# Kernel tuning notes

Measured on AMD Instinct MI355X. Metric: run time of the kernel, lower is better.

Reference implementation:

```python
import jax, jax.numpy as jnp
import numpy as np

N_NODES = 10000
N_EDGES = 320000
N_GRAPHS = 64
K = 10
IN_C, HID_C, OUT_C = 128, 256, 128


def setup_inputs() -> dict:
    key = jax.random.key(0)
    ks = jax.random.split(key, 10)
    s_in = 1.0 / np.sqrt(IN_C)
    s_hid = 1.0 / np.sqrt(HID_C)
    return {
        "x": jax.random.normal(ks[0], (N_NODES, IN_C), jnp.float32),
        "W0": jax.random.normal(ks[1], (K, IN_C, HID_C), jnp.float32) * s_in,
        "b0": jnp.zeros((HID_C,), jnp.float32),
        "W1": jax.random.normal(ks[2], (K, HID_C, HID_C), jnp.float32) * s_hid,
        "b1": jnp.zeros((HID_C,), jnp.float32),
        "W2": jax.random.normal(ks[3], (K, HID_C, HID_C), jnp.float32) * s_hid,
        "b2": jnp.zeros((HID_C,), jnp.float32),
        "W_out": jax.random.normal(ks[4], (HID_C, OUT_C), jnp.float32) * s_hid,
        "b_out": jnp.zeros((OUT_C,), jnp.float32),
        "edge_index": jax.random.randint(ks[5], (2, N_EDGES), 0, N_NODES, jnp.int64),
        "batch": jnp.sort(jax.random.randint(ks[6], (N_NODES,), 0, N_GRAPHS, jnp.int64)),
    }


def _edge_norm(src, dst, n):
    # Scaled Laplacian L_hat = 2L/lambda_max - I with lambda_max=2 and sym norm
    # => L_hat = -D^{-1/2} A D^{-1/2} (diagonal entries cancel to 0).
    deg = jnp.zeros((n,), jnp.float32).at[src].add(1.0)
    dis = jnp.where(deg > 0, jax.lax.rsqrt(jnp.maximum(deg, 1.0)), 0.0)
    return -dis[src] * dis[dst]


def _propagate(x, src, dst, w, n):
    # message = w * x[src], aggregated by sum at dst
    return jax.ops.segment_sum(w[:, None] * x[src], dst, num_segments=n)


def _cheb_conv(x, src, dst, w, W, b, n):
    # Tx_0 = x; Tx_1 = L_hat x; Tx_k = 2 L_hat Tx_{k-1} - Tx_{k-2}
    K_ = W.shape[0]
    Tx0 = x
    out = Tx0 @ W[0]
    Tx1 = _propagate(Tx0, src, dst, w, n)
    out = out + Tx1 @ W[1]
    for k in range(2, K_):
        Tx2 = 2.0 * _propagate(Tx1, src, dst, w, n) - Tx0
        out = out + Tx2 @ W[k]
        Tx0, Tx1 = Tx1, Tx2
    return out + b


def reference(x, W0, b0, W1, b1, W2, b2, W_out, b_out, edge_index, batch):
    n = x.shape[0]
    src, dst = edge_index[0], edge_index[1]
    w = _edge_norm(src, dst, n)
    # 3 ChebConv layers, each followed by ReLU (norm=None, dropout=0)
    h = jax.nn.relu(_cheb_conv(x, src, dst, w, W0, b0, n))
    h = jax.nn.relu(_cheb_conv(h, src, dst, w, W1, b1, n))
    h = jax.nn.relu(_cheb_conv(h, src, dst, w, W2, b2, n))
    # global_mean_pool over batch ids
    sums = jax.ops.segment_sum(h, batch, num_segments=N_GRAPHS)
    cnts = jax.ops.segment_sum(jnp.ones((n,), h.dtype), batch, num_segments=N_GRAPHS)
    pooled = sums / jnp.maximum(cnts, 1.0)[:, None]
    return pooled @ W_out + b_out
```

## Files before the change

### kernel.cpp

```cpp
#include <hip/hip_runtime.h>
#include <cstdint>
#include <cstddef>

#define N_NODES 10000
#define N_EDGES 320000
#define N_GRAPHS 64
#define KCHEB 10
#define C_IN 128
#define C_HID 256
#define C_OUTC 128
#define POOL_CHUNK 40

static inline size_t align_up(size_t v, size_t a){ return (v + a - 1) / a * a; }

typedef __attribute__((ext_vector_type(8))) _Float16 half8;
typedef __attribute__((ext_vector_type(2))) _Float16 h2;
typedef __attribute__((ext_vector_type(4))) float f32x4;


__global__ void k_deg(const int* __restrict__ src, const int* __restrict__ dst,
                      int* __restrict__ deg, int* __restrict__ indeg){
  int e = blockIdx.x*blockDim.x + threadIdx.x;
  if(e < N_EDGES){
    atomicAdd(&deg[src[e]], 1);
    atomicAdd(&indeg[dst[e]], 1);
  }
}

__global__ __launch_bounds__(1024) void k_scan(const int* __restrict__ cnt,
                                               int* __restrict__ offs,
                                               int* __restrict__ cursor,
                                               const int* __restrict__ deg,
                                               float* __restrict__ dis){
  __shared__ int part[1024];
  const int n = N_NODES;
  const int CH = (n + 1023) / 1024;
  int tid = threadIdx.x;
  int base = tid * CH;
  int s = 0;
  for(int i = 0; i < CH; i++){
    int idx = base + i;
    if(idx < n){
      s += cnt[idx];
      int d = deg[idx];
      dis[idx] = d > 0 ? rsqrtf((float)d) : 0.f;
    }
  }
  part[tid] = s;
  __syncthreads();
  for(int off = 1; off < 1024; off <<= 1){
    int v = (tid >= off) ? part[tid - off] : 0;
    __syncthreads();
    part[tid] += v;
    __syncthreads();
  }
  int run = (tid == 0) ? 0 : part[tid - 1];
  for(int i = 0; i < CH; i++){
    int idx = base + i;
    if(idx < n){
      offs[idx] = run;
      cursor[idx] = run;
      run += cnt[idx];
    }
  }
  if(tid == 1023) offs[n] = part[1023];
}

__global__ void k_scatter(const int* __restrict__ src, const int* __restrict__ dst,
                          const float* __restrict__ dis, int* __restrict__ cursor,
                          int* __restrict__ csr_s, unsigned* __restrict__ csr_wp){
  int e = blockIdx.x*blockDim.x + threadIdx.x;
  if(e < N_EDGES){
    int s = src[e], d = dst[e];
    float w = -dis[s] * dis[d];
    unsigned short wb = __builtin_bit_cast(unsigned short, (_Float16)w);
    int p = atomicAdd(&cursor[d], 1);
    csr_s[p] = s;
    csr_wp[p] = (unsigned)wb * 0x00010001u;
  }
}

__global__ __launch_bounds__(128) void k_gbounds(const int* __restrict__ batch,
                                                 int* __restrict__ gstart,
                                                 int* __restrict__ gcnt){
  int g = threadIdx.x;
  if(g <= N_GRAPHS){
    int lo = 0, hi = N_NODES;
    while(lo < hi){
      int mid = (lo + hi) >> 1;
      if(batch[mid] < g) lo = mid + 1; else hi = mid;
    }
    gstart[g] = lo;
  }
  __syncthreads();
  if(g < N_GRAPHS) gcnt[g] = gstart[g + 1] - gstart[g];
}


__device__ inline void hfma4(h2* a, uint4 v, unsigned wbits){
  h2 w2 = __builtin_bit_cast(h2, wbits);
  a[0] += __builtin_bit_cast(h2, v.x) * w2;
  a[1] += __builtin_bit_cast(h2, v.y) * w2;
  a[2] += __builtin_bit_cast(h2, v.z) * w2;
  a[3] += __builtin_bit_cast(h2, v.w) * w2;
}

__global__ __launch_bounds__(256) void k_prop256h(const _Float16* __restrict__ Xb,
                                                  const _Float16* __restrict__ Pb,
                                                  _Float16* __restrict__ tx,
                                                  const int* __restrict__ csr_s,
                                                  const unsigned* __restrict__ csr_wp,
                                                  const int* __restrict__ offs,
                                                  float alpha){
  const int stride  = KCHEB * C_HID;
  const int strideB = stride * 2;
  int bid  = blockIdx.x;
  int half = (bid >> 2) & 1;
  int lh   = (bid >> 3) * 4 + (bid & 3);
  int l15  = threadIdx.x & 15;
  int lane = threadIdx.x & 63;
  int b16  = lane & 48;
  int e8   = l15 & 7;
  int node = lh * 16 + (threadIdx.x >> 4);
  if(node >= N_NODES) return;
  int j0 = offs[node], j1 = offs[node + 1];
  h2 a[4] = {};
  const char* __restrict__ gbase = (const char*)Xb + (half * (C_HID/2) + l15 * 8) * 2;
  int j = j0;
  int sv = 0; unsigned wv = 0;
  bool have = (j + 7 < j1);
  if(have){ sv = csr_s[j + e8] * strideB; wv = csr_wp[j + e8]; }
  while(have){
    int jn = j + 8;
    bool more = (jn + 7 < j1);
    int sv2 = 0; unsigned wv2 = 0;
    if(more){ sv2 = csr_s[jn + e8] * strideB; wv2 = csr_wp[jn + e8]; }
    uint4 v[8];
#pragma unroll
    for(int i = 0; i < 8; i++){
      int si = __shfl(sv, b16 + i);
      v[i] = *(const uint4*)(gbase + si);
    }
#pragma unroll
    for(int i = 0; i < 8; i++){
      unsigned wi = (unsigned)__shfl((int)wv, b16 + i);
      hfma4(a, v[i], wi);
    }
    sv = sv2; wv = wv2; j = jn; have = more;
  }
  for(; j < j1; j++){
    int si = csr_s[j] * strideB;
    uint4 v0 = *(const uint4*)(gbase + si);
    hfma4(a, v0, csr_wp[j]);
  }
  _Float16 ah = (_Float16)alpha;
  h2 al = {ah, ah};
  h2 r[4];
#pragma unroll
  for(int i = 0; i < 4; i++) r[i] = a[i] * al;
  size_t off = (size_t)node * stride + half * (C_HID/2) + l15 * 8;
  if(Pb){
    uint4 pv = *(const uint4*)(Pb + off);
    r[0] -= __builtin_bit_cast(h2, pv.x);
    r[1] -= __builtin_bit_cast(h2, pv.y);
    r[2] -= __builtin_bit_cast(h2, pv.z);
    r[3] -= __builtin_bit_cast(h2, pv.w);
  }
  uint4 ob;
  ob.x = __builtin_bit_cast(unsigned, r[0]);
  ob.y = __builtin_bit_cast(unsigned, r[1]);
  ob.z = __builtin_bit_cast(unsigned, r[2]);
  ob.w = __builtin_bit_cast(unsigned, r[3]);
  *(uint4*)(tx + off) = ob;
}

__global__ __launch_bounds__(256) void k_prop128(const _Float16* __restrict__ Xb,
                                                 const _Float16* __restrict__ Pb,
                                                 _Float16* __restrict__ tx,
                                                 const int* __restrict__ csr_s,
                                                 const unsigned* __restrict__ csr_wp,
                                                 const int* __restrict__ offs,
                                                 float alpha){
  const int stride  = KCHEB * C_IN;
  const int strideB = stride * 2;
  int hl   = threadIdx.x & 31;
  int b32  = threadIdx.x & 32;
  int e8   = hl & 7;
  int node = blockIdx.x * 8 + (threadIdx.x >> 5);
  int j0 = offs[node], j1 = offs[node + 1];
  h2 a[2] = {};
  const char* __restrict__ gbase = (const char*)Xb + hl * 8;
  int j = j0;
  int sv = 0; unsigned wv = 0;
  bool have = (j + 7 < j1);
  if(have){ sv = csr_s[j + e8] * strideB; wv = csr_wp[j + e8]; }
  while(have){
    int jn = j + 8;
    bool more = (jn + 7 < j1);
    int sv2 = 0; unsigned wv2 = 0;
    if(more){ sv2 = csr_s[jn + e8] * strideB; wv2 = csr_wp[jn + e8]; }
    uint2 v[8];
#pragma unroll
    for(int i = 0; i < 8; i++){
      int si = __shfl(sv, b32 + i);
      v[i] = *(const uint2*)(gbase + si);
    }
#pragma unroll
    for(int i = 0; i < 8; i++){
      unsigned wi = (unsigned)__shfl((int)wv, b32 + i);
      h2 w2 = __builtin_bit_cast(h2, wi);
      a[0] += __builtin_bit_cast(h2, v[i].x) * w2;
      a[1] += __builtin_bit_cast(h2, v[i].y) * w2;
    }
    sv = sv2; wv = wv2; j = jn; have = more;
  }
  for(; j < j1; j++){
    int si = csr_s[j] * strideB;
    h2 w2 = __builtin_bit_cast(h2, csr_wp[j]);
    uint2 v0 = *(const uint2*)(gbase + si);
    a[0] += __builtin_bit_cast(h2, v0.x) * w2;
    a[1] += __builtin_bit_cast(h2, v0.y) * w2;
  }
  _Float16 ah = (_Float16)alpha;
  h2 al = {ah, ah};
  h2 r0 = a[0] * al, r1 = a[1] * al;
  size_t off = (size_t)node * stride + hl * 4;
  if(Pb){
    uint2 pv = *(const uint2*)(Pb + off);
    r0 -= __builtin_bit_cast(h2, pv.x);
    r1 -= __builtin_bit_cast(h2, pv.y);
  }
  uint2 ob;
  ob.x = __builtin_bit_cast(unsigned, r0);
  ob.y = __builtin_bit_cast(unsigned, r1);
  *(uint2*)(tx + off) = ob;
}

template<int C>
__global__ void k_f2h(const float* __restrict__ X, _Float16* __restrict__ tx,
                      int tx_stride){
  int idx = blockIdx.x * blockDim.x + threadIdx.x;
  const int GPR = C / 4;
  if(idx < N_NODES * GPR){
    int r = idx / GPR;
    int c = (idx - r * GPR) * 4;
    float4 v = *(const float4*)(X + (size_t)r * C + c);
    h2 p0 = {(_Float16)v.x, (_Float16)v.y};
    h2 p1 = {(_Float16)v.z, (_Float16)v.w};
    uint2 ob;
    ob.x = __builtin_bit_cast(unsigned, p0);
    ob.y = __builtin_bit_cast(unsigned, p1);
    *(uint2*)(tx + (size_t)r * tx_stride + c) = ob;
  }
}

__global__ __launch_bounds__(256) void k_wt3t(const float* __restrict__ W0, _Float16* __restrict__ WT0,
                                              const float* __restrict__ W1, _Float16* __restrict__ WT1,
                                              const float* __restrict__ W2, _Float16* __restrict__ WT2){
  __shared__ float t[32][33];
  int b = blockIdx.x;
  const float* W; _Float16* WT; int R; int tb;
  if(b < 320){ W = W0; WT = WT0; R = 1280; tb = b; }
  else if(b < 960){ W = W1; WT = WT1; R = 2560; tb = b - 320; }
  else { W = W2; WT = WT2; R = 2560; tb = b - 960; }
  int tr = tb >> 3, tc = tb & 7;
  int tx = threadIdx.x & 31, ty = threadIdx.x >> 5;
#pragma unroll
  for(int i = 0; i < 4; i++){
    int r = tr * 32 + ty + 8 * i;
    t[ty + 8 * i][tx] = W[(size_t)r * 256 + tc * 32 + tx];
  }
  __syncthreads();
#pragma unroll
  for(int i = 0; i < 4; i++){
    int o = tc * 32 + ty + 8 * i;
    WT[(size_t)o * R + tr * 32 + tx] = (_Float16)t[tx][ty + 8 * i];
  }
}


__global__ __launch_bounds__(256) void k_gemm_f(const _Float16* __restrict__ A,
                                                const _Float16* __restrict__ BT,
                                                const float* __restrict__ bias,
                                                float* __restrict__ H,
                                                _Float16* __restrict__ tx2,
                                                int M, int Ktot){
  int b = blockIdx.x;
  int xcd = b & 7;
  int l = b >> 3;
  int m = xcd + 8 * (l >> 2);
  int n = l & 3;
  if(m * 128 >= M) return;
  int row0 = m * 128, col0 = n * 64;

  __shared__ short As[2][128 * 64];
  __shared__ short Bs[2][64 * 64];
  int tid = threadIdx.x;
  int lane = tid & 63;
  int wave = tid >> 6;
  int l15 = lane & 15;
  int quad = lane >> 4;
  int wm = (wave & 1) * 64;
  int wn = (wave >> 1) * 32;

  int ar[4], ag[4], asw[4], agr[4];
#pragma unroll
  for(int i = 0; i < 4; i++){
    int e = tid + 256 * i;
    ar[i] = e >> 3; ag[i] = e & 7;
    agr[i] = row0 + ar[i];
    asw[i] = ar[i] * 64 + ((ag[i] ^ (ar[i] & 7)) * 8);
  }
  int br[2], bg[2], bsw[2];
#pragma unroll
  for(int i = 0; i < 2; i++){
    int e = tid + 256 * i;
    br[i] = e >> 3; bg[i] = e & 7;
    bsw[i] = br[i] * 64 + ((bg[i] ^ (br[i] & 7)) * 8);
  }

  f32x4 acc[4][2] = {};
  uint4 av[4], bv[2];

  auto load = [&](int k0){
#pragma unroll
    for(int i = 0; i < 4; i++)
      av[i] = (agr[i] < M) ? *(const uint4*)(A + (size_t)agr[i] * Ktot + k0 + ag[i] * 8)
                           : make_uint4(0u, 0u, 0u, 0u);
#pragma unroll
    for(int i = 0; i < 2; i++)
      bv[i] = *(const uint4*)(BT + (size_t)(col0 + br[i]) * Ktot + k0 + bg[i] * 8);
  };
  auto stor = [&](int buf){
#pragma unroll
    for(int i = 0; i < 4; i++) *(uint4*)(&As[buf][asw[i]]) = av[i];
#pragma unroll
    for(int i = 0; i < 2; i++) *(uint4*)(&Bs[buf][bsw[i]]) = bv[i];
  };

  load(0);
  stor(0);
  __syncthreads();
  int nk = Ktot >> 6;
  for(int it = 0; it < nk; it++){
    int cur = it & 1;
    if(it + 1 < nk) load((it + 1) << 6);
#pragma unroll
    for(int kk = 0; kk < 64; kk += 32){
      int g = (kk >> 3) + quad;
      half8 a[4], bb[2];
#pragma unroll
      for(int mi = 0; mi < 4; mi++){
        int r = wm + mi * 16 + l15;
        a[mi] = *(const half8*)(&As[cur][r * 64 + ((g ^ (r & 7)) * 8)]);
      }
#pragma unroll
      for(int ni = 0; ni < 2; ni++){
        int nn = wn + ni * 16 + l15;
        bb[ni] = *(const half8*)(&Bs[cur][nn * 64 + ((g ^ (nn & 7)) * 8)]);
      }
#pragma unroll
      for(int mi = 0; mi < 4; mi++)
#pragma unroll
        for(int ni = 0; ni < 2; ni++)
          acc[mi][ni] = __builtin_amdgcn_mfma_f32_16x16x32_f16(a[mi], bb[ni], acc[mi][ni], 0, 0, 0);
    }
    if(it + 1 < nk){
      stor(cur ^ 1);
      __syncthreads();
    }
  }

  const int K256 = KCHEB * C_HID;
#pragma unroll
  for(int mi = 0; mi < 4; mi++){
#pragma unroll
    for(int ni = 0; ni < 2; ni++){
      int gcol = col0 + wn + ni * 16 + l15;
      float bvv = bias[gcol];
#pragma unroll
      for(int r = 0; r < 4; r++){
        int grow = row0 + wm + mi * 16 + quad * 4 + r;
        if(grow < M){
          float v = fmaxf(acc[mi][ni][r] + bvv, 0.f);
          if(tx2) tx2[(size_t)grow * K256 + gcol] = (_Float16)v;
          else    H[(size_t)grow * C_HID + gcol] = v;
        }
      }
    }
  }
}


__global__ __launch_bounds__(256) void k_pool2(const float* __restrict__ h,
                                               const int* __restrict__ batch,
                                               float* __restrict__ gsum){
  int c  = threadIdx.x;
  int n0 = blockIdx.x * POOL_CHUNK;
  int n1 = n0 + POOL_CHUNK;
  if(n1 > N_NODES) n1 = N_NODES;
  if(n0 >= n1) return;
  float acc = 0.f;
  int cur = batch[n0];
  for(int n = n0; n < n1; n++){
    int g = batch[n];
    if(g != cur){
      atomicAdd(&gsum[cur * C_HID + c], acc);
      acc = 0.f;
      cur = g;
    }
    acc += h[(size_t)n * C_HID + c];
  }
  atomicAdd(&gsum[cur * C_HID + c], acc);
}

__global__ __launch_bounds__(128) void k_final(const float* __restrict__ gsum,
                                               const int* __restrict__ gcnt,
                                               const float* __restrict__ Wout,
                                               const float* __restrict__ bout,
                                               float* __restrict__ out){
  int g = blockIdx.x;
  int o = threadIdx.x;
  float inv = 1.f / fmaxf((float)gcnt[g], 1.f);
  float acc = bout[o];
  for(int c = 0; c < C_HID; c++) acc += gsum[g * C_HID + c] * inv * Wout[c * C_OUTC + o];
  out[g * C_OUTC + o] = acc;
}


extern "C" void kernel_launch(void* const* d_in, const int* in_sizes, int n_in,
                              void* d_out, int out_size, void* d_ws, size_t ws_size,
                              hipStream_t stream){
  const float* x    = (const float*)d_in[0];
  const float* W0   = (const float*)d_in[1];
  const float* b0   = (const float*)d_in[2];
  const float* W1   = (const float*)d_in[3];
  const float* b1   = (const float*)d_in[4];
  const float* W2   = (const float*)d_in[5];
  const float* b2   = (const float*)d_in[6];
  const float* Wout = (const float*)d_in[7];
  const float* bout = (const float*)d_in[8];
  const int*   ei   = (const int*)d_in[9];
  const int*   batch= (const int*)d_in[10];
  const int* src = ei;
  const int* dst = ei + N_EDGES;
  float* out = (float*)d_out;

  char* p = (char*)d_ws;
  auto alloc = [&](size_t bytes)->char*{ char* r = p; p += align_up(bytes, 256); return r; };

  int*   deg    = (int*)  alloc(N_NODES * 4);
  int*   indeg  = (int*)  alloc(N_NODES * 4);
  int*   offs   = (int*)  alloc((N_NODES + 1) * 4);
  int*   cursor = (int*)  alloc(N_NODES * 4);
  float* dis    = (float*)alloc(N_NODES * 4);
  int*   csr_s  = (int*)  alloc(N_EDGES * 4);
  unsigned* csr_wp = (unsigned*)alloc(N_EDGES * 4);
  int*   gcnt   = (int*)  alloc(N_GRAPHS * 4);
  int*   gstart = (int*)  alloc((N_GRAPHS + 1) * 4);
  float* gsum   = (float*)alloc(N_GRAPHS * C_HID * 4);

  const size_t txBytes = (size_t)N_NODES * (KCHEB * C_HID) * 2;
  _Float16* txP = (_Float16*)alloc(txBytes);
  _Float16* txQ = (_Float16*)alloc(txBytes);
  _Float16* WT0 = (_Float16*)alloc((size_t)KCHEB * C_IN  * C_HID * 2);
  _Float16* WT1 = (_Float16*)alloc((size_t)KCHEB * C_HID * C_HID * 2);
  _Float16* WT2 = (_Float16*)alloc((size_t)KCHEB * C_HID * C_HID * 2);
  float* Hb = (float*)alloc((size_t)N_NODES * C_HID * 4);

  hipMemsetAsync(deg,   0, N_NODES * 4, stream);
  hipMemsetAsync(indeg, 0, N_NODES * 4, stream);
  hipMemsetAsync(gsum,  0, N_GRAPHS * C_HID * 4, stream);

  const int TB = 256;
  int egrid = (N_EDGES + TB - 1) / TB;

  k_deg<<<egrid, TB, 0, stream>>>(src, dst, deg, indeg);
  k_scan<<<1, 1024, 0, stream>>>(indeg, offs, cursor, deg, dis);
  k_scatter<<<egrid, TB, 0, stream>>>(src, dst, dis, cursor, csr_s, csr_wp);
  k_gbounds<<<1, 128, 0, stream>>>(batch, gstart, gcnt);
  k_wt3t<<<1600, 256, 0, stream>>>(W0, WT0, W1, WT1, W2, WT2);

  const int K128 = KCHEB * C_IN;
  const int K256 = KCHEB * C_HID;
  const int GEMM_BLOCKS = 320;
  const int PROP_H_BLOCKS = 1256;
  const int PROP_1_BLOCKS = N_NODES / 8;

  {
    int ng = N_NODES * (C_IN / 4);
    k_f2h<C_IN><<<(ng + TB - 1) / TB, TB, 0, stream>>>(x, txP, K128);
    for(int k = 1; k < KCHEB; k++){
      const _Float16* Xb = txP + (size_t)(k - 1) * C_IN;
      const _Float16* Pb = (k >= 2) ? txP + (size_t)(k - 2) * C_IN : nullptr;
      _Float16* tx = txP + (size_t)k * C_IN;
      k_prop128<<<PROP_1_BLOCKS, 256, 0, stream>>>(Xb, Pb, tx, csr_s, csr_wp, offs,
                                                   k == 1 ? 1.f : 2.f);
    }
    k_gemm_f<<<GEMM_BLOCKS, 256, 0, stream>>>(txP, WT0, b0, nullptr, txQ, N_NODES, K128);
  }

  {
    for(int k = 1; k < KCHEB; k++){
      const _Float16* Xb = txQ + (size_t)(k - 1) * C_HID;
      const _Float16* Pb = (k >= 2) ? txQ + (size_t)(k - 2) * C_HID : nullptr;
      _Float16* tx = txQ + (size_t)k * C_HID;
      k_prop256h<<<PROP_H_BLOCKS, 256, 0, stream>>>(Xb, Pb, tx, csr_s, csr_wp, offs,
                                                    k == 1 ? 1.f : 2.f);
    }
    k_gemm_f<<<GEMM_BLOCKS, 256, 0, stream>>>(txQ, WT1, b1, nullptr, txP, N_NODES, K256);
  }

  {
    for(int k = 1; k < KCHEB; k++){
      const _Float16* Xb = txP + (size_t)(k - 1) * C_HID;
      const _Float16* Pb = (k >= 2) ? txP + (size_t)(k - 2) * C_HID : nullptr;
      _Float16* tx = txP + (size_t)k * C_HID;
      k_prop256h<<<PROP_H_BLOCKS, 256, 0, stream>>>(Xb, Pb, tx, csr_s, csr_wp, offs,
                                                    k == 1 ? 1.f : 2.f);
    }
    k_gemm_f<<<GEMM_BLOCKS, 256, 0, stream>>>(txP, WT2, b2, Hb, nullptr, N_NODES, K256);
  }

  k_pool2<<<(N_NODES + POOL_CHUNK - 1) / POOL_CHUNK, 256, 0, stream>>>(Hb, batch, gsum);
  k_final<<<N_GRAPHS, C_OUTC, 0, stream>>>(gsum, gcnt, Wout, bout, out);
}
```

Baseline: 722.1 us.

## Sort nodes by in-degree for propagation and halve GEMM row tile

The scan kernel now builds a degree histogram in shared memory and produces a permutation that orders nodes by descending in-degree. Both propagation kernels process nodes in that order, so wavefronts get neighbours with similar edge counts and waste fewer idle cycles. Separately, the GEMM tile shrinks from 128 to 64 rows and the block count doubles, to give the CUs more parallel work. The cost is an extra indirection load per node, scattered output writes, and less reuse per GEMM block.

```diff
diff --git a/kernel.cpp b/kernel.cpp
--- a/kernel.cpp
+++ b/kernel.cpp
@@ -31,12 +31,16 @@
                                                int* __restrict__ offs,
                                                int* __restrict__ cursor,
                                                const int* __restrict__ deg,
-                                               float* __restrict__ dis){
+                                               float* __restrict__ dis,
+                                               int* __restrict__ perm){
   __shared__ int part[1024];
+  __shared__ int hist[256];
+  __shared__ int hoff[256];
   const int n = N_NODES;
   const int CH = (n + 1023) / 1024;
   int tid = threadIdx.x;
   int base = tid * CH;
+  if(tid < 256) hist[tid] = 0;
   int s = 0;
   for(int i = 0; i < CH; i++){
     int idx = base + i;
@@ -61,9 +65,25 @@
       offs[idx] = run;
       cursor[idx] = run;
       run += cnt[idx];
+      int d = cnt[idx]; if(d > 255) d = 255;
+      atomicAdd(&hist[d], 1);
     }
   }
   if(tid == 1023) offs[n] = part[1023];
+  __syncthreads();
+  if(tid == 0){
+    int r2 = 0;
+    for(int d = 255; d >= 0; d--){ hoff[d] = r2; r2 += hist[d]; }
+  }
+  __syncthreads();
+  for(int i = 0; i < CH; i++){
+    int idx = base + i;
+    if(idx < n){
+      int d = cnt[idx]; if(d > 255) d = 255;
+      int p0 = atomicAdd(&hoff[d], 1);
+      perm[p0] = idx;
+    }
+  }
 }
 
 __global__ void k_scatter(const int* __restrict__ src, const int* __restrict__ dst,
@@ -111,6 +131,7 @@
                                                   const int* __restrict__ csr_s,
                                                   const unsigned* __restrict__ csr_wp,
                                                   const int* __restrict__ offs,
+                                                  const int* __restrict__ perm,
                                                   float alpha){
   const int stride  = KCHEB * C_HID;
   const int strideB = stride * 2;
@@ -121,8 +142,9 @@
   int lane = threadIdx.x & 63;
   int b16  = lane & 48;
   int e8   = l15 & 7;
-  int node = lh * 16 + (threadIdx.x >> 4);
-  if(node >= N_NODES) return;
+  int nidx = lh * 16 + (threadIdx.x >> 4);
+  if(nidx >= N_NODES) return;
+  int node = perm[nidx];
   int j0 = offs[node], j1 = offs[node + 1];
   h2 a[4] = {};
   const char* __restrict__ gbase = (const char*)Xb + (half * (C_HID/2) + l15 * 8) * 2;
@@ -180,13 +202,14 @@
                                                  const int* __restrict__ csr_s,
                                                  const unsigned* __restrict__ csr_wp,
                                                  const int* __restrict__ offs,
+                                                 const int* __restrict__ perm,
                                                  float alpha){
   const int stride  = KCHEB * C_IN;
   const int strideB = stride * 2;
   int hl   = threadIdx.x & 31;
   int b32  = threadIdx.x & 32;
   int e8   = hl & 7;
-  int node = blockIdx.x * 8 + (threadIdx.x >> 5);
+  int node = perm[blockIdx.x * 8 + (threadIdx.x >> 5)];
   int j0 = offs[node], j1 = offs[node + 1];
   h2 a[2] = {};
   const char* __restrict__ gbase = (const char*)Xb + hl * 8;
@@ -290,52 +313,42 @@
   int l = b >> 3;
   int m = xcd + 8 * (l >> 2);
   int n = l & 3;
-  if(m * 128 >= M) return;
-  int row0 = m * 128, col0 = n * 64;
-
-  __shared__ short As[2][128 * 64];
+  if(m * 64 >= M) return;
+  int row0 = m * 64, col0 = n * 64;
+
+  __shared__ short As[2][64 * 64];
   __shared__ short Bs[2][64 * 64];
   int tid = threadIdx.x;
   int lane = tid & 63;
   int wave = tid >> 6;
   int l15 = lane & 15;
   int quad = lane >> 4;
-  int wm = (wave & 1) * 64;
+  int wm = (wave & 1) * 32;
   int wn = (wave >> 1) * 32;
 
-  int ar[4], ag[4], asw[4], agr[4];
-#pragma unroll
-  for(int i = 0; i < 4; i++){
-    int e = tid + 256 * i;
-    ar[i] = e >> 3; ag[i] = e & 7;
-    agr[i] = row0 + ar[i];
-    asw[i] = ar[i] * 64 + ((ag[i] ^ (ar[i] & 7)) * 8);
-  }
-  int br[2], bg[2], bsw[2];
-#pragma unroll
-  for(int i = 0; i < 2; i++){
-    int e = tid + 256 * i;
-    br[i] = e >> 3; bg[i] = e & 7;
-    bsw[i] = br[i] * 64 + ((bg[i] ^ (br[i] & 7)) * 8);
-  }
-
-  f32x4 acc[4][2] = {};
-  uint4 av[4], bv[2];
+  int e0 = tid, e1 = tid + 256;
+  int r0 = e0 >> 3, g0 = e0 & 7;
+  int r1 = e1 >> 3, g1 = e1 & 7;
+  int gr0 = row0 + r0, gr1 = row0 + r1;
+  int sa0 = r0 * 64 + ((g0 ^ (r0 & 7)) * 8);
+  int sa1 = r1 * 64 + ((g1 ^ (r1 & 7)) * 8);
+
+  f32x4 acc[2][2] = {};
+  uint4 av0, av1, bv0, bv1;
 
   auto load = [&](int k0){
-#pragma unroll
-    for(int i = 0; i < 4; i++)
-      av[i] = (agr[i] < M) ? *(const uint4*)(A + (size_t)agr[i] * Ktot + k0 + ag[i] * 8)
-                           : make_uint4(0u, 0u, 0u, 0u);
-#pragma unroll
-    for(int i = 0; i < 2; i++)
-      bv[i] = *(const uint4*)(BT + (size_t)(col0 + br[i]) * Ktot + k0 + bg[i] * 8);
+    av0 = (gr0 < M) ? *(const uint4*)(A + (size_t)gr0 * Ktot + k0 + g0 * 8)
+                    : make_uint4(0u, 0u, 0u, 0u);
+    av1 = (gr1 < M) ? *(const uint4*)(A + (size_t)gr1 * Ktot + k0 + g1 * 8)
+                    : make_uint4(0u, 0u, 0u, 0u);
+    bv0 = *(const uint4*)(BT + (size_t)(col0 + r0) * Ktot + k0 + g0 * 8);
+    bv1 = *(const uint4*)(BT + (size_t)(col0 + r1) * Ktot + k0 + g1 * 8);
   };
   auto stor = [&](int buf){
-#pragma unroll
-    for(int i = 0; i < 4; i++) *(uint4*)(&As[buf][asw[i]]) = av[i];
-#pragma unroll
-    for(int i = 0; i < 2; i++) *(uint4*)(&Bs[buf][bsw[i]]) = bv[i];
+    *(uint4*)(&As[buf][sa0]) = av0;
+    *(uint4*)(&As[buf][sa1]) = av1;
+    *(uint4*)(&Bs[buf][sa0]) = bv0;
+    *(uint4*)(&Bs[buf][sa1]) = bv1;
   };
 
   load(0);
@@ -348,9 +361,9 @@
 #pragma unroll
     for(int kk = 0; kk < 64; kk += 32){
       int g = (kk >> 3) + quad;
-      half8 a[4], bb[2];
-#pragma unroll
-      for(int mi = 0; mi < 4; mi++){
+      half8 a[2], bb[2];
+#pragma unroll
+      for(int mi = 0; mi < 2; mi++){
         int r = wm + mi * 16 + l15;
         a[mi] = *(const half8*)(&As[cur][r * 64 + ((g ^ (r & 7)) * 8)]);
       }
@@ -360,7 +373,7 @@
         bb[ni] = *(const half8*)(&Bs[cur][nn * 64 + ((g ^ (nn & 7)) * 8)]);
       }
 #pragma unroll
-      for(int mi = 0; mi < 4; mi++)
+      for(int mi = 0; mi < 2; mi++)
 #pragma unroll
         for(int ni = 0; ni < 2; ni++)
           acc[mi][ni] = __builtin_amdgcn_mfma_f32_16x16x32_f16(a[mi], bb[ni], acc[mi][ni], 0, 0, 0);
@@ -373,16 +386,16 @@
 
   const int K256 = KCHEB * C_HID;
 #pragma unroll
-  for(int mi = 0; mi < 4; mi++){
+  for(int mi = 0; mi < 2; mi++){
 #pragma unroll
     for(int ni = 0; ni < 2; ni++){
       int gcol = col0 + wn + ni * 16 + l15;
-      float bvv = bias[gcol];
+      float bv = bias[gcol];
 #pragma unroll
       for(int r = 0; r < 4; r++){
         int grow = row0 + wm + mi * 16 + quad * 4 + r;
         if(grow < M){
-          float v = fmaxf(acc[mi][ni][r] + bvv, 0.f);
+          float v = fmaxf(acc[mi][ni][r] + bv, 0.f);
           if(tx2) tx2[(size_t)grow * K256 + gcol] = (_Float16)v;
           else    H[(size_t)grow * C_HID + gcol] = v;
         }
@@ -454,6 +467,7 @@
   int*   offs   = (int*)  alloc((N_NODES + 1) * 4);
   int*   cursor = (int*)  alloc(N_NODES * 4);
   float* dis    = (float*)alloc(N_NODES * 4);
+  int*   perm   = (int*)  alloc(N_NODES * 4);
   int*   csr_s  = (int*)  alloc(N_EDGES * 4);
   unsigned* csr_wp = (unsigned*)alloc(N_EDGES * 4);
   int*   gcnt   = (int*)  alloc(N_GRAPHS * 4);
@@ -476,14 +490,14 @@
   int egrid = (N_EDGES + TB - 1) / TB;
 
   k_deg<<<egrid, TB, 0, stream>>>(src, dst, deg, indeg);
-  k_scan<<<1, 1024, 0, stream>>>(indeg, offs, cursor, deg, dis);
+  k_scan<<<1, 1024, 0, stream>>>(indeg, offs, cursor, deg, dis, perm);
   k_scatter<<<egrid, TB, 0, stream>>>(src, dst, dis, cursor, csr_s, csr_wp);
   k_gbounds<<<1, 128, 0, stream>>>(batch, gstart, gcnt);
   k_wt3t<<<1600, 256, 0, stream>>>(W0, WT0, W1, WT1, W2, WT2);
 
   const int K128 = KCHEB * C_IN;
   const int K256 = KCHEB * C_HID;
-  const int GEMM_BLOCKS = 320;
+  const int GEMM_BLOCKS = 640;
   const int PROP_H_BLOCKS = 1256;
   const int PROP_1_BLOCKS = N_NODES / 8;
 
@@ -494,7 +508,7 @@
       const _Float16* Xb = txP + (size_t)(k - 1) * C_IN;
       const _Float16* Pb = (k >= 2) ? txP + (size_t)(k - 2) * C_IN : nullptr;
       _Float16* tx = txP + (size_t)k * C_IN;
-      k_prop128<<<PROP_1_BLOCKS, 256, 0, stream>>>(Xb, Pb, tx, csr_s, csr_wp, offs,
+      k_prop128<<<PROP_1_BLOCKS, 256, 0, stream>>>(Xb, Pb, tx, csr_s, csr_wp, offs, perm,
                                                    k == 1 ? 1.f : 2.f);
     }
     k_gemm_f<<<GEMM_BLOCKS, 256, 0, stream>>>(txP, WT0, b0, nullptr, txQ, N_NODES, K128);
@@ -505,7 +519,7 @@
       const _Float16* Xb = txQ + (size_t)(k - 1) * C_HID;
       const _Float16* Pb = (k >= 2) ? txQ + (size_t)(k - 2) * C_HID : nullptr;
       _Float16* tx = txQ + (size_t)k * C_HID;
-      k_prop256h<<<PROP_H_BLOCKS, 256, 0, stream>>>(Xb, Pb, tx, csr_s, csr_wp, offs,
+      k_prop256h<<<PROP_H_BLOCKS, 256, 0, stream>>>(Xb, Pb, tx, csr_s, csr_wp, offs, perm,
                                                     k == 1 ? 1.f : 2.f);
     }
     k_gemm_f<<<GEMM_BLOCKS, 256, 0, stream>>>(txQ, WT1, b1, nullptr, txP, N_NODES, K256);
@@ -516,7 +530,7 @@
       const _Float16* Xb = txP + (size_t)(k - 1) * C_HID;
       const _Float16* Pb = (k >= 2) ? txP + (size_t)(k - 2) * C_HID : nullptr;
       _Float16* tx = txP + (size_t)k * C_HID;
-      k_prop256h<<<PROP_H_BLOCKS, 256, 0, stream>>>(Xb, Pb, tx, csr_s, csr_wp, offs,
+      k_prop256h<<<PROP_H_BLOCKS, 256, 0, stream>>>(Xb, Pb, tx, csr_s, csr_wp, offs, perm,
                                                     k == 1 ? 1.f : 2.f);
     }
     k_gemm_f<<<GEMM_BLOCKS, 256, 0, stream>>>(txP, WT2, b2, Hb, nullptr, N_NODES, K256);
```

After: 626.8 us. -13.2%, faster.
